# Performance work log

Hardware: AMD Instinct MI355X
Metric: run time of the kernel (lower is better)

Reference implementation:

```python
import jax, jax.numpy as jnp
import numpy as np

B, C, D, H, W = 2, 512, 32, 32, 32
L, CTX = 256, 768
NH, HD, G = 8, 64, 8
EPS = 1e-5


def group_norm(x, w, b):
    Bb, Cc, Dd, Hh, Ww = x.shape
    xg = x.reshape(Bb, G, Cc // G, Dd, Hh, Ww)
    mu = xg.mean(axis=(2, 3, 4, 5), keepdims=True)
    var = xg.var(axis=(2, 3, 4, 5), keepdims=True)
    xn = ((xg - mu) * jax.lax.rsqrt(var + EPS)).reshape(Bb, Cc, Dd, Hh, Ww)
    return xn * w[None, :, None, None, None] + b[None, :, None, None, None]


def layer_norm(x, w, b):
    mu = x.mean(axis=-1, keepdims=True)
    var = x.var(axis=-1, keepdims=True)
    return (x - mu) * jax.lax.rsqrt(var + EPS) * w + b


def setup_inputs() -> dict:
    key = jax.random.key(0)
    ks = jax.random.split(key, 8)
    s = 0.02  # weight init scale
    return {
        "x": jax.random.normal(ks[0], (B, C, D, H, W), jnp.float32),
        "context": jax.random.normal(ks[1], (B, L, CTX), jnp.float32),
        "gn_w": jnp.ones((C,), jnp.float32),
        "gn_b": jnp.zeros((C,), jnp.float32),
        "ln_w": jnp.ones((CTX,), jnp.float32),
        "ln_b": jnp.zeros((CTX,), jnp.float32),
        "q_w": jax.random.normal(ks[2], (C, C), jnp.float32) * s,
        "q_b": jnp.zeros((C,), jnp.float32),
        "k_w": jax.random.normal(ks[3], (C, CTX), jnp.float32) * s,
        "k_b": jnp.zeros((C,), jnp.float32),
        "v_w": jax.random.normal(ks[4], (C, CTX), jnp.float32) * s,
        "v_b": jnp.zeros((C,), jnp.float32),
        "proj_w": jax.random.normal(ks[5], (C, C), jnp.float32) * s,
        "proj_b": jnp.zeros((C,), jnp.float32),
    }


def reference(x, context, gn_w, gn_b, ln_w, ln_b, q_w, q_b, k_w, k_b, v_w, v_b, proj_w, proj_b):
    Bb, Cc, Dd, Hh, Ww = x.shape
    S = Dd * Hh * Ww
    h = group_norm(x, gn_w, gn_b)
    ctx = layer_norm(context, ln_w, ln_b)
    # 1x1 Conv3d == per-voxel linear over channels
    q = jnp.einsum('oc,bcdhw->bodhw', q_w, h) + q_b[None, :, None, None, None]
    q = q.reshape(Bb, NH, HD, S)                                        # (b,h,e,s)
    k = (ctx @ k_w.T + k_b).reshape(Bb, L, NH, HD).transpose(0, 2, 1, 3)  # (b,h,l,e)
    v = (ctx @ v_w.T + v_b).reshape(Bb, L, NH, HD).transpose(0, 2, 1, 3)  # (b,h,l,e)
    scale = HD ** -0.5
    attn = jnp.einsum('bhes,bhle->bhsl', q, k) * scale                  # (b,h,S,L)
    attn = jax.nn.softmax(attn, axis=-1)
    out = jnp.einsum('bhsl,bhle->bhes', attn, v).reshape(Bb, Cc, Dd, Hh, Ww)
    out = jnp.einsum('oc,bcdhw->bodhw', proj_w, out) + proj_b[None, :, None, None, None]
    return out + x
```

## Files before the change

### kernel.cpp

```cpp
#include <hip/hip_runtime.h>

typedef unsigned short u16;
typedef unsigned int u32;
typedef __attribute__((ext_vector_type(4))) float f32x4;
typedef __attribute__((ext_vector_type(8))) short bf16x8;
typedef __attribute__((ext_vector_type(8))) u16 u16x8;
typedef __attribute__((ext_vector_type(4))) u16 u16x4;
typedef __attribute__((ext_vector_type(4))) u32 u32x4;

#define DEVI __device__ __forceinline__

constexpr int C_ = 512, S_ = 32768, L_ = 256, CTX_ = 768;

DEVI u16 f2b(float f) {
    union { float f; unsigned u; } x; x.f = f;
    unsigned r = x.u + 0x7fffu + ((x.u >> 16) & 1u);
    return (u16)(r >> 16);
}

DEVI f32x4 mfma16(bf16x8 a, bf16x8 b, f32x4 c) {
    return __builtin_amdgcn_mfma_f32_16x16x32_bf16(a, b, c, 0, 0, 0);
}

DEVI void gload16(const void* g, void* l) {
    __builtin_amdgcn_global_load_lds(
        (const __attribute__((address_space(1))) void*)g,
        (__attribute__((address_space(3))) void*)l, 16, 0, 0);
}

DEVI u32 cvtpk(float lo, float hi) {
    u32 d;
    asm("v_cvt_pk_bf16_f32 %0, %1, %2" : "=v"(d) : "v"(lo), "v"(hi));
    return d;
}
DEVI void pl32(u32& a, u32& b) {
    asm volatile("v_permlane32_swap_b32 %0, %1" : "+v"(a), "+v"(b));
}
DEVI void pl16(u32& a, u32& b) {
    asm volatile("v_permlane16_swap_b32 %0, %1" : "+v"(a), "+v"(b));
}

__global__ __launch_bounds__(256) void cvt_w(
    const float* __restrict__ a0, const float* __restrict__ a1,
    const float* __restrict__ a2, const float* __restrict__ a3,
    u16* __restrict__ o0, u16* __restrict__ o1,
    u16* __restrict__ o2, u16* __restrict__ o3)
{
    int which = blockIdx.y;
    const float* src = which == 0 ? a0 : which == 1 ? a1 : which == 2 ? a2 : a3;
    u16* dst = which == 0 ? o0 : which == 1 ? o1 : which == 2 ? o2 : o3;
    int n4 = (which == 1 || which == 2) ? (512 * 768 / 4) : (512 * 512 / 4);
    int i = blockIdx.x * 256 + threadIdx.x;
    if (i < n4) {
        float4 v = ((const float4*)src)[i];
        u16x4 o; o[0] = f2b(v.x); o[1] = f2b(v.y); o[2] = f2b(v.z); o[3] = f2b(v.w);
        ((u16x4*)dst)[i] = o;
    }
}

__global__ __launch_bounds__(256) void gn_partial(const float* __restrict__ x,
                                                  float* __restrict__ part)
{
    const int bg = blockIdx.y, blk = blockIdx.x, tid = threadIdx.x;
    const float* base = x + (size_t)bg * 64 * S_ + (size_t)blk * 1024 + tid * 4;
    float s1 = 0.f, s2 = 0.f;
    for (int c = 0; c < 64; ++c) {
        float4 v = *(const float4*)(base + (size_t)c * S_);
        s1 += v.x + v.y + v.z + v.w;
        s2 += v.x * v.x + v.y * v.y + v.z * v.z + v.w * v.w;
    }
    for (int m = 1; m < 64; m <<= 1) { s1 += __shfl_xor(s1, m); s2 += __shfl_xor(s2, m); }
    __shared__ float a1[4], a2[4];
    int w = tid >> 6, lane = tid & 63;
    if (lane == 0) { a1[w] = s1; a2[w] = s2; }
    __syncthreads();
    if (tid == 0) {
        part[(bg * 32 + blk) * 2 + 0] = a1[0] + a1[1] + a1[2] + a1[3];
        part[(bg * 32 + blk) * 2 + 1] = a2[0] + a2[1] + a2[2] + a2[3];
    }
}

__global__ __launch_bounds__(64) void gn_final(const float* __restrict__ part,
                                               float* __restrict__ stats)
{
    int bg = blockIdx.x, tid = threadIdx.x;
    float s1 = tid < 32 ? part[(bg * 32 + tid) * 2] : 0.f;
    float s2 = tid < 32 ? part[(bg * 32 + tid) * 2 + 1] : 0.f;
    for (int m = 1; m < 32; m <<= 1) { s1 += __shfl_xor(s1, m); s2 += __shfl_xor(s2, m); }
    if (tid == 0) {
        const float invN = 1.0f / (64.0f * (float)S_);
        float mu = s1 * invN, var = s2 * invN - mu * mu;
        stats[bg * 2] = mu;
        stats[bg * 2 + 1] = rsqrtf(var + 1e-5f);
    }
}

__global__ __launch_bounds__(256) void gn_apply(
    const float* __restrict__ x, const float* __restrict__ stats,
    const float* __restrict__ gw, const float* __restrict__ gb,
    u16* __restrict__ ht)
{
    __shared__ float tile[64][65];
    const int tid = threadIdx.x, sl = tid & 63, c4 = tid >> 6;
    const int s0 = blockIdx.x * 64, c0 = blockIdx.y * 64, b = blockIdx.z;
    const int bg = b * 8 + (c0 >> 6);
    const float mu = stats[bg * 2], rstd = stats[bg * 2 + 1];
#pragma unroll
    for (int i = 0; i < 16; ++i) {
        int cl = c4 * 16 + i;
        float wv = gw[c0 + cl], bv = gb[c0 + cl];
        float v = x[((size_t)(b * C_ + c0 + cl)) * S_ + s0 + sl];
        tile[sl][cl] = (v - mu) * rstd * wv + bv;
    }
    __syncthreads();
#pragma unroll
    for (int rep = 0; rep < 2; ++rep) {
        int task = rep * 256 + tid;
        int so = task >> 3, cb = task & 7;
        u16x8 o;
#pragma unroll
        for (int j = 0; j < 8; ++j) o[j] = f2b(tile[so][cb * 8 + j]);
        *(u16x8*)&ht[((size_t)(b * S_ + s0 + so)) * C_ + c0 + cb * 8] = o;
    }
}

__global__ __launch_bounds__(256) void ln_ctx(
    const float* __restrict__ ctx, const float* __restrict__ lw,
    const float* __restrict__ lb, u16* __restrict__ cn)
{
    const int row = blockIdx.x, tid = threadIdx.x;
    const float* p = ctx + (size_t)row * CTX_;
    float v0 = p[tid], v1 = p[tid + 256], v2 = p[tid + 512];
    float s1 = v0 + v1 + v2, s2 = v0 * v0 + v1 * v1 + v2 * v2;
    for (int m = 1; m < 64; m <<= 1) { s1 += __shfl_xor(s1, m); s2 += __shfl_xor(s2, m); }
    __shared__ float a1[4], a2[4];
    int w = tid >> 6, lane = tid & 63;
    if (lane == 0) { a1[w] = s1; a2[w] = s2; }
    __syncthreads();
    s1 = a1[0] + a1[1] + a1[2] + a1[3];
    s2 = a2[0] + a2[1] + a2[2] + a2[3];
    const float invN = 1.0f / 768.0f;
    float mu = s1 * invN, rstd = rsqrtf(s2 * invN - mu * mu + 1e-5f);
    u16* o = cn + (size_t)row * CTX_;
    o[tid]       = f2b((v0 - mu) * rstd * lw[tid]       + lb[tid]);
    o[tid + 256] = f2b((v1 - mu) * rstd * lw[tid + 256] + lb[tid + 256]);
    o[tid + 512] = f2b((v2 - mu) * rstd * lw[tid + 512] + lb[tid + 512]);
}

template <int MODE, bool SWAP>
__global__ __launch_bounds__(256, 4) void gemm_nt(
    const u16* __restrict__ A, const u16* __restrict__ Bp,
    const float* __restrict__ bias, void* __restrict__ outp,
    const float* __restrict__ resid, int K, int ldo,
    size_t aStride, size_t bStride, size_t oStride, float scale,
    const u16* __restrict__ Bp2, const float* __restrict__ bias2,
    void* __restrict__ outp2)
{
    __shared__ __align__(16) u16 lA[2][4096];
    __shared__ __align__(16) u16 lB[2][4096];
    const int tid = threadIdx.x;
    const int w = tid >> 6, lane = tid & 63;
    const int g = lane >> 4, r = lane & 15;

    const int nx = gridDim.x, nxy = nx * gridDim.y;
    const int raw = blockIdx.x + nx * blockIdx.y;
    const int tile = (raw & 7) * (nxy >> 3) + (raw >> 3);
    const int bx = tile % nx, by = tile / nx;
    const int m0 = (SWAP ? by : bx) * 128, n0 = (SWAP ? bx : by) * 128;
    const int z = blockIdx.z;
    A += (size_t)z * aStride;
    const u16* Bsel = Bp;
    if constexpr (MODE == 3) { if (z) Bsel = Bp2; }
    Bsel += (size_t)z * bStride;

    const int l8 = lane & 7, lh = lane >> 3;
    const int u_ = l8 ^ lh;
    const int mro = (lh << 1) + (u_ >> 2);
    const int kco = (u_ & 3) * 8;
    const int wr = w >> 1, wc = w & 1;
    const int nt = K >> 5;

    f32x4 acc[4][4];
#pragma unroll
    for (int m = 0; m < 4; ++m)
#pragma unroll
        for (int n = 0; n < 4; ++n) acc[m][n] = f32x4{0.f, 0.f, 0.f, 0.f};

#define STAGE_T(t, bi_) {                                                      \
    size_t ko_ = (size_t)((t) * 32 + kco);                                     \
    _Pragma("unroll")                                                          \
    for (int j = 0; j < 2; ++j) {                                              \
        int grow_ = w * 32 + j * 16 + mro;                                     \
        gload16(A + (size_t)(m0 + grow_) * K + ko_,                            \
                &lA[bi_][(w * 16 + j * 8) << 6]);                              \
        gload16(Bsel + (size_t)(n0 + grow_) * K + ko_,                         \
                &lB[bi_][(w * 16 + j * 8) << 6]);                              \
    } }

    STAGE_T(0, 0);
    __syncthreads();

    for (int t = 0; t < nt; ++t) {
        const int cur = t & 1;
        if (t + 1 < nt) STAGE_T(t + 1, cur ^ 1);
        bf16x8 af[4], bf_[4];
#pragma unroll
        for (int m = 0; m < 4; ++m) {
            int row = wr * 32 + m * 8 + (r >> 1);
            int slot = (((r & 1) << 2) + g) ^ ((r >> 1) & 7);
            af[m] = *(const bf16x8*)&lA[cur][(row << 6) + (slot << 3)];
        }
#pragma unroll
        for (int n = 0; n < 4; ++n) {
            int row = wc * 32 + n * 8 + (r >> 1);
            int slot = (((r & 1) << 2) + g) ^ ((r >> 1) & 7);
            bf_[n] = *(const bf16x8*)&lB[cur][(row << 6) + (slot << 3)];
        }
#pragma unroll
        for (int m = 0; m < 4; ++m)
#pragma unroll
            for (int n = 0; n < 4; ++n)
                acc[m][n] = mfma16(bf_[n], af[m], acc[m][n]);
        __syncthreads();
    }
#undef STAGE_T

    if constexpr (MODE == 0) {
        u16* ob = (u16*)outp + (size_t)z * oStride;
#pragma unroll
        for (int m = 0; m < 4; ++m) {
            int gm = m0 + wr * 64 + m * 16 + r;
#pragma unroll
            for (int n = 0; n < 4; ++n) {
                int gn0 = n0 + wc * 64 + n * 16 + g * 4;
                float4 bn = *(const float4*)&bias[gn0];
                u32 w0 = cvtpk(acc[m][n][0] * scale + bn.x * scale,
                               acc[m][n][1] * scale + bn.y * scale);
                u32 w1 = cvtpk(acc[m][n][2] * scale + bn.z * scale,
                               acc[m][n][3] * scale + bn.w * scale);
                *(uint2*)&ob[(size_t)gm * ldo + gn0] = make_uint2(w0, w1);
            }
        }
    } else if constexpr (MODE == 2) {
        float* of = (float*)outp + (size_t)z * oStride;
        const float* rs = resid + (size_t)z * oStride;
#pragma unroll
        for (int m = 0; m < 4; ++m) {
            int gm = m0 + wr * 64 + m * 16 + r;
            float bm = bias[gm];
#pragma unroll
            for (int n = 0; n < 4; ++n) {
                int gn0 = n0 + wc * 64 + n * 16 + g * 4;
                size_t idx = (size_t)gm * ldo + gn0;
                float4 rv = *(const float4*)&rs[idx];
                float4 o4;
                o4.x = acc[m][n][0] + bm + rv.x;
                o4.y = acc[m][n][1] + bm + rv.y;
                o4.z = acc[m][n][2] + bm + rv.z;
                o4.w = acc[m][n][3] + bm + rv.w;
                *(float4*)&of[idx] = o4;
            }
        }
    } else if constexpr (MODE == 3) {
        if (z == 0) {
            u16* ob = (u16*)outp;
#pragma unroll
            for (int m = 0; m < 4; ++m) {
                int gm = m0 + wr * 64 + m * 16 + r;
#pragma unroll
                for (int n = 0; n < 4; ++n) {
                    int gn0 = n0 + wc * 64 + n * 16 + g * 4;
                    float4 bn = *(const float4*)&bias[gn0];
                    u32 w0 = cvtpk(acc[m][n][0] + bn.x, acc[m][n][1] + bn.y);
                    u32 w1 = cvtpk(acc[m][n][2] + bn.z, acc[m][n][3] + bn.w);
                    *(uint2*)&ob[(size_t)gm * ldo + gn0] = make_uint2(w0, w1);
                }
            }
        } else {
            u16* ob = (u16*)outp2;
#pragma unroll
            for (int m = 0; m < 4; ++m) {
                int gm = m0 + wr * 64 + m * 16 + r;
                int bb = gm >> 8, l = gm & 255;
#pragma unroll
                for (int n = 0; n < 4; ++n) {
                    int gn0 = n0 + wc * 64 + n * 16 + g * 4;
#pragma unroll
                    for (int i = 0; i < 4; ++i)
                        ob[((size_t)(bb * 512 + gn0 + i)) * 256 + l] =
                            f2b(acc[m][n][i] + bias2[gn0 + i]);
                }
            }
        }
    }
}

__global__ __launch_bounds__(256, 2) void attn_kernel(
    const u16* __restrict__ q, const u16* __restrict__ kk,
    const u16* __restrict__ vv, u16* __restrict__ ao)
{
    __shared__ __align__(16) u16 sm[32768];
    const int tid = threadIdx.x;
    const int w = tid >> 6, lane = tid & 63;
    const int g = lane >> 4, r = lane & 15;
    const int bh = blockIdx.y, b = bh >> 3, h = bh & 7;
    const int s0 = blockIdx.x * 128;

    {
        const u16* kbase = kk + ((size_t)b * L_) * C_ + h * 64;
#pragma unroll
        for (int j = 0; j < 8; ++j) {
            int idx = j * 256 + tid;
            int l = idx >> 3, ch = idx & 7;
            u16x8 val = *(const u16x8*)(kbase + (size_t)l * C_ + ch * 8);
            *(u16x8*)&sm[l * 64 + ((ch ^ (l & 7)) << 3)] = val;
        }
        const u16* vbase = vv + ((size_t)bh * 64) * 256;
#pragma unroll
        for (int j = 0; j < 8; ++j) {
            int idx = j * 256 + tid;
            int e = idx >> 5, ch = idx & 31;
            u16x8 val = *(const u16x8*)(vbase + (size_t)e * 256 + ch * 8);
            *(u16x8*)&sm[16384 + e * 256 + ((ch ^ (e & 7)) << 3)] = val;
        }
    }

    const int sw = s0 + w * 32;
    bf16x8 qf[2][2];
#pragma unroll
    for (int m = 0; m < 2; ++m)
#pragma unroll
        for (int kt = 0; kt < 2; ++kt)
            qf[m][kt] = *(const bf16x8*)(q + ((size_t)(b * S_ + sw + m * 16 + r)) * C_
                                         + h * 64 + kt * 32 + g * 8);
    __syncthreads();

    f32x4 accs[2][16];
#pragma unroll
    for (int m = 0; m < 2; ++m)
#pragma unroll
        for (int n = 0; n < 16; ++n) accs[m][n] = f32x4{0.f, 0.f, 0.f, 0.f};
    __builtin_amdgcn_s_setprio(1);
#pragma unroll
    for (int n = 0; n < 16; ++n) {
#pragma unroll
        for (int kt = 0; kt < 2; ++kt) {
            int c = kt * 4 + g;
            bf16x8 kf = *(const bf16x8*)&sm[(n * 16 + r) * 64 + ((c ^ (r & 7)) << 3)];
#pragma unroll
            for (int m = 0; m < 2; ++m) accs[m][n] = mfma16(kf, qf[m][kt], accs[m][n]);
        }
    }
    __builtin_amdgcn_s_setprio(0);

    float inv[2];
#pragma unroll
    for (int m = 0; m < 2; ++m) {
        float mx = accs[m][0][0];
#pragma unroll
        for (int n = 0; n < 16; ++n)
#pragma unroll
            for (int i = 0; i < 4; ++i) mx = fmaxf(mx, accs[m][n][i]);
        mx = fmaxf(mx, __shfl_xor(mx, 16));
        mx = fmaxf(mx, __shfl_xor(mx, 32));
        float sum = 0.f;
#pragma unroll
        for (int n = 0; n < 16; ++n)
#pragma unroll
            for (int i = 0; i < 4; ++i) {
                float e = __expf(accs[m][n][i] - mx);
                accs[m][n][i] = e; sum += e;
            }
        sum += __shfl_xor(sum, 16);
        sum += __shfl_xor(sum, 32);
        inv[m] = 1.0f / sum;
    }

    f32x4 acco[2][4];
#pragma unroll
    for (int m = 0; m < 2; ++m)
#pragma unroll
        for (int n = 0; n < 4; ++n) acco[m][n] = f32x4{0.f, 0.f, 0.f, 0.f};

#pragma unroll
    for (int c = 0; c < 8; ++c) {
        bf16x8 pa[2];
#pragma unroll
        for (int m = 0; m < 2; ++m) {
            u32 x0 = cvtpk(accs[m][2 * c][0] * inv[m], accs[m][2 * c][1] * inv[m]);
            u32 x1 = cvtpk(accs[m][2 * c][2] * inv[m], accs[m][2 * c][3] * inv[m]);
            u32 y0 = cvtpk(accs[m][2 * c + 1][0] * inv[m], accs[m][2 * c + 1][1] * inv[m]);
            u32 y1 = cvtpk(accs[m][2 * c + 1][2] * inv[m], accs[m][2 * c + 1][3] * inv[m]);
            pl32(x0, y0);
            pl32(x1, y1);
            pl16(x0, y0);
            pl16(x1, y1);
            u32x4 pw; pw[0] = x0; pw[1] = x1; pw[2] = y0; pw[3] = y1;
            pa[m] = *(bf16x8*)&pw;
        }
        bf16x8 vf[4];
#pragma unroll
        for (int n = 0; n < 4; ++n) {
            int e = n * 16 + r;
            vf[n] = *(const bf16x8*)&sm[16384 + e * 256 + (((c * 4 + g) ^ (r & 7)) << 3)];
        }
        __builtin_amdgcn_s_setprio(1);
#pragma unroll
        for (int m = 0; m < 2; ++m)
#pragma unroll
            for (int n = 0; n < 4; ++n)
                acco[m][n] = mfma16(vf[n], pa[m], acco[m][n]);
        __builtin_amdgcn_s_setprio(0);
    }

#pragma unroll
    for (int m = 0; m < 2; ++m) {
        const size_t rowb = ((size_t)(b * S_ + sw + m * 16 + r)) * C_ + h * 64;
#pragma unroll
        for (int n = 0; n < 4; ++n) {
            u32 w0 = cvtpk(acco[m][n][0], acco[m][n][1]);
            u32 w1 = cvtpk(acco[m][n][2], acco[m][n][3]);
            *(uint2*)&ao[rowb + n * 16 + g * 4] = make_uint2(w0, w1);
        }
    }
}

extern "C" void kernel_launch(void* const* d_in, const int* in_sizes, int n_in,
                              void* d_out, int out_size, void* d_ws, size_t ws_size,
                              hipStream_t stream)
{
    (void)in_sizes; (void)n_in; (void)out_size; (void)ws_size;
    const float* x    = (const float*)d_in[0];
    const float* ctx  = (const float*)d_in[1];
    const float* gn_w = (const float*)d_in[2];
    const float* gn_b = (const float*)d_in[3];
    const float* ln_w = (const float*)d_in[4];
    const float* ln_b = (const float*)d_in[5];
    const float* q_w  = (const float*)d_in[6];
    const float* q_b  = (const float*)d_in[7];
    const float* k_w  = (const float*)d_in[8];
    const float* k_b  = (const float*)d_in[9];
    const float* v_w  = (const float*)d_in[10];
    const float* v_b  = (const float*)d_in[11];
    const float* p_w  = (const float*)d_in[12];
    const float* p_b  = (const float*)d_in[13];
    float* out = (float*)d_out;

    char* ws = (char*)d_ws;
    constexpr size_t WS_WQ   = 0;
    constexpr size_t WS_WK   = WS_WQ + (size_t)512 * 512 * 2;
    constexpr size_t WS_WV   = WS_WK + (size_t)512 * 768 * 2;
    constexpr size_t WS_WP   = WS_WV + (size_t)512 * 768 * 2;
    constexpr size_t WS_PART = WS_WP + (size_t)512 * 512 * 2;
    constexpr size_t WS_STAT = WS_PART + (size_t)16 * 64 * 2 * 4;
    constexpr size_t WS_CTXN = WS_STAT + 256;
    constexpr size_t WS_K    = WS_CTXN + (size_t)512 * 768 * 2;
    constexpr size_t WS_V    = WS_K + (size_t)2 * 8 * 256 * 64 * 2;
    constexpr size_t WS_Q    = WS_V + (size_t)2 * 8 * 256 * 64 * 2;
    constexpr size_t WS_H    = WS_Q + (size_t)2 * 32768 * 512 * 2;

    u16* wq = (u16*)(ws + WS_WQ);
    u16* wk = (u16*)(ws + WS_WK);
    u16* wv = (u16*)(ws + WS_WV);
    u16* wp = (u16*)(ws + WS_WP);
    float* part  = (float*)(ws + WS_PART);
    float* stats = (float*)(ws + WS_STAT);
    u16* ctxn = (u16*)(ws + WS_CTXN);
    u16* kt   = (u16*)(ws + WS_K);
    u16* vt   = (u16*)(ws + WS_V);
    u16* qt   = (u16*)(ws + WS_Q);
    u16* ht   = (u16*)(ws + WS_H);
    u16* ao   = ht;

    const size_t bsc = (size_t)S_ * C_;

    cvt_w<<<dim3(384, 4), 256, 0, stream>>>(q_w, k_w, v_w, p_w, wq, wk, wv, wp);
    gn_partial<<<dim3(32, 16), 256, 0, stream>>>(x, part);
    gn_final<<<16, 64, 0, stream>>>(part, stats);
    gn_apply<<<dim3(512, 8, 2), 256, 0, stream>>>(x, stats, gn_w, gn_b, ht);
    ln_ctx<<<512, 256, 0, stream>>>(ctx, ln_w, ln_b, ctxn);
    gemm_nt<0, true><<<dim3(4, 256, 2), 256, 0, stream>>>(
        ht, wq, q_b, qt, nullptr, 512, 512, bsc, 0, bsc, 0.125f,
        nullptr, nullptr, nullptr);
    gemm_nt<3, false><<<dim3(4, 4, 2), 256, 0, stream>>>(
        ctxn, wk, k_b, kt, nullptr, 768, 512, 0, 0, 0, 1.0f,
        wv, v_b, vt);
    attn_kernel<<<dim3(256, 16), 256, 0, stream>>>(qt, kt, vt, ao);
    gemm_nt<2, false><<<dim3(4, 256, 2), 256, 0, stream>>>(
        wp, ao, p_b, out, x, 512, S_, 0, bsc, bsc, 1.0f,
        nullptr, nullptr, nullptr);
}
```

Baseline: 282.1 us.

## Fuse GroupNorm apply into Q projection GEMM A-operand load

Removes the gn_apply kernel that wrote a normalized, transposed bf16 copy of x. The Q GEMM now reads fp32 x directly and applies per-channel scale and shift coefficients from a tiny gn_coef kernel. It then converts to bf16 and writes the swizzled LDS tile, with the global loads issued ahead and the LDS writes done after the MFMAs. This saves a full write and re-read of the 32 MB intermediate, but the GEMM now loads fp32 data with register staging instead of async gload16, which may cost latency hiding.

```diff
diff --git a/kernel.cpp b/kernel.cpp
--- a/kernel.cpp
+++ b/kernel.cpp
@@ -95,33 +95,17 @@
     }
 }
 
-__global__ __launch_bounds__(256) void gn_apply(
-    const float* __restrict__ x, const float* __restrict__ stats,
-    const float* __restrict__ gw, const float* __restrict__ gb,
-    u16* __restrict__ ht)
-{
-    __shared__ float tile[64][65];
-    const int tid = threadIdx.x, sl = tid & 63, c4 = tid >> 6;
-    const int s0 = blockIdx.x * 64, c0 = blockIdx.y * 64, b = blockIdx.z;
-    const int bg = b * 8 + (c0 >> 6);
-    const float mu = stats[bg * 2], rstd = stats[bg * 2 + 1];
-#pragma unroll
-    for (int i = 0; i < 16; ++i) {
-        int cl = c4 * 16 + i;
-        float wv = gw[c0 + cl], bv = gb[c0 + cl];
-        float v = x[((size_t)(b * C_ + c0 + cl)) * S_ + s0 + sl];
-        tile[sl][cl] = (v - mu) * rstd * wv + bv;
-    }
-    __syncthreads();
-#pragma unroll
-    for (int rep = 0; rep < 2; ++rep) {
-        int task = rep * 256 + tid;
-        int so = task >> 3, cb = task & 7;
-        u16x8 o;
-#pragma unroll
-        for (int j = 0; j < 8; ++j) o[j] = f2b(tile[so][cb * 8 + j]);
-        *(u16x8*)&ht[((size_t)(b * S_ + s0 + so)) * C_ + c0 + cb * 8] = o;
-    }
+__global__ __launch_bounds__(256) void gn_coef(
+    const float* __restrict__ stats, const float* __restrict__ gw,
+    const float* __restrict__ gb, float* __restrict__ ca, float* __restrict__ cb)
+{
+    int i = blockIdx.x * 256 + threadIdx.x;
+    int z = i >> 9, c = i & 511;
+    int bg = z * 8 + (c >> 6);
+    float mu = stats[bg * 2], rs = stats[bg * 2 + 1];
+    float a = rs * gw[c];
+    ca[i] = a;
+    cb[i] = gb[c] - mu * a;
 }
 
 __global__ __launch_bounds__(256) void ln_ctx(
@@ -186,23 +170,76 @@
 #pragma unroll
         for (int n = 0; n < 4; ++n) acc[m][n] = f32x4{0.f, 0.f, 0.f, 0.f};
 
-#define STAGE_T(t, bi_) {                                                      \
+#define STAGE_B(t, bi_) {                                                      \
+    size_t ko_ = (size_t)((t) * 32 + kco);                                     \
+    _Pragma("unroll")                                                          \
+    for (int j = 0; j < 2; ++j) {                                              \
+        int grow_ = w * 32 + j * 16 + mro;                                     \
+        gload16(Bsel + (size_t)(n0 + grow_) * K + ko_,                         \
+                &lB[bi_][(w * 16 + j * 8) << 6]);                              \
+    } }
+
+#define STAGE_A(t, bi_) {                                                      \
     size_t ko_ = (size_t)((t) * 32 + kco);                                     \
     _Pragma("unroll")                                                          \
     for (int j = 0; j < 2; ++j) {                                              \
         int grow_ = w * 32 + j * 16 + mro;                                     \
         gload16(A + (size_t)(m0 + grow_) * K + ko_,                            \
                 &lA[bi_][(w * 16 + j * 8) << 6]);                              \
-        gload16(Bsel + (size_t)(n0 + grow_) * K + ko_,                         \
-                &lB[bi_][(w * 16 + j * 8) << 6]);                              \
     } }
 
-    STAGE_T(0, 0);
+    const float* xA = nullptr;
+    const float* cAp = nullptr;
+    const float* cBp = nullptr;
+    int cp2 = 0, sb = 0, zc = 0;
+    f32x4 a00{}, a01{}, a10{}, a11{};
+    float2 ka{}, kb{};
+    if constexpr (MODE == 4) {
+        xA = resid + (size_t)z * ((size_t)C_ * S_);
+        cAp = bias2;
+        cBp = (const float*)outp2;
+        cp2 = (tid >> 4) * 2;
+        sb = (tid & 15) * 8;
+        zc = z * 512;
+    }
+
+#define LOAD_A4(t) {                                                           \
+    int c0n_ = (t) * 32 + cp2;                                                 \
+    const float* r0_ = xA + (size_t)c0n_ * S_ + m0 + sb;                       \
+    a00 = *(const f32x4*)r0_;  a01 = *(const f32x4*)(r0_ + 4);                 \
+    a10 = *(const f32x4*)(r0_ + S_); a11 = *(const f32x4*)(r0_ + S_ + 4);      \
+    ka = *(const float2*)&cAp[zc + c0n_];                                      \
+    kb = *(const float2*)&cBp[zc + c0n_]; }
+
+#define WRITE_A4(bi_) {                                                        \
+    _Pragma("unroll")                                                          \
+    for (int j = 0; j < 8; ++j) {                                              \
+        float v0_ = ((j < 4) ? a00[j] : a01[j - 4]) * ka.x + kb.x;             \
+        float v1_ = ((j < 4) ? a10[j] : a11[j - 4]) * ka.y + kb.y;             \
+        int mm_ = sb + j;                                                      \
+        int idx_ = ((mm_ >> 1) << 6)                                           \
+            + (((((mm_ & 1) << 2) + (cp2 >> 3)) ^ ((mm_ >> 1) & 7)) << 3)      \
+            + (cp2 & 7);                                                       \
+        *(u32*)&lA[bi_][idx_] = cvtpk(v0_, v1_);                               \
+    } }
+
+    if constexpr (MODE == 4) {
+        STAGE_B(0, 0);
+        LOAD_A4(0);
+        WRITE_A4(0);
+    } else {
+        STAGE_A(0, 0);
+        STAGE_B(0, 0);
+    }
     __syncthreads();
 
     for (int t = 0; t < nt; ++t) {
         const int cur = t & 1;
-        if (t + 1 < nt) STAGE_T(t + 1, cur ^ 1);
+        if (t + 1 < nt) {
+            STAGE_B(t + 1, cur ^ 1);
+            if constexpr (MODE == 4) { LOAD_A4(t + 1); }
+            else                     { STAGE_A(t + 1, cur ^ 1); }
+        }
         bf16x8 af[4], bf_[4];
 #pragma unroll
         for (int m = 0; m < 4; ++m) {
@@ -221,11 +258,15 @@
 #pragma unroll
             for (int n = 0; n < 4; ++n)
                 acc[m][n] = mfma16(bf_[n], af[m], acc[m][n]);
+        if constexpr (MODE == 4) { if (t + 1 < nt) WRITE_A4(cur ^ 1); }
         __syncthreads();
     }
-#undef STAGE_T
-
-    if constexpr (MODE == 0) {
+#undef STAGE_A
+#undef STAGE_B
+#undef LOAD_A4
+#undef WRITE_A4
+
+    if constexpr (MODE == 0 || MODE == 4) {
         u16* ob = (u16*)outp + (size_t)z * oStride;
 #pragma unroll
         for (int m = 0; m < 4; ++m) {
@@ -453,7 +494,9 @@
     constexpr size_t WS_WP   = WS_WV + (size_t)512 * 768 * 2;
     constexpr size_t WS_PART = WS_WP + (size_t)512 * 512 * 2;
     constexpr size_t WS_STAT = WS_PART + (size_t)16 * 64 * 2 * 4;
-    constexpr size_t WS_CTXN = WS_STAT + 256;
+    constexpr size_t WS_CA   = WS_STAT + 256;
+    constexpr size_t WS_CB   = WS_CA + 4096;
+    constexpr size_t WS_CTXN = WS_CB + 4096;
     constexpr size_t WS_K    = WS_CTXN + (size_t)512 * 768 * 2;
     constexpr size_t WS_V    = WS_K + (size_t)2 * 8 * 256 * 64 * 2;
     constexpr size_t WS_Q    = WS_V + (size_t)2 * 8 * 256 * 64 * 2;
@@ -465,23 +508,24 @@
     u16* wp = (u16*)(ws + WS_WP);
     float* part  = (float*)(ws + WS_PART);
     float* stats = (float*)(ws + WS_STAT);
+    float* coefA = (float*)(ws + WS_CA);
+    float* coefB = (float*)(ws + WS_CB);
     u16* ctxn = (u16*)(ws + WS_CTXN);
     u16* kt   = (u16*)(ws + WS_K);
     u16* vt   = (u16*)(ws + WS_V);
     u16* qt   = (u16*)(ws + WS_Q);
-    u16* ht   = (u16*)(ws + WS_H);
-    u16* ao   = ht;
+    u16* ao   = (u16*)(ws + WS_H);
 
     const size_t bsc = (size_t)S_ * C_;
 
     cvt_w<<<dim3(384, 4), 256, 0, stream>>>(q_w, k_w, v_w, p_w, wq, wk, wv, wp);
     gn_partial<<<dim3(32, 16), 256, 0, stream>>>(x, part);
     gn_final<<<16, 64, 0, stream>>>(part, stats);
-    gn_apply<<<dim3(512, 8, 2), 256, 0, stream>>>(x, stats, gn_w, gn_b, ht);
+    gn_coef<<<4, 256, 0, stream>>>(stats, gn_w, gn_b, coefA, coefB);
     ln_ctx<<<512, 256, 0, stream>>>(ctx, ln_w, ln_b, ctxn);
-    gemm_nt<0, true><<<dim3(4, 256, 2), 256, 0, stream>>>(
-        ht, wq, q_b, qt, nullptr, 512, 512, bsc, 0, bsc, 0.125f,
-        nullptr, nullptr, nullptr);
+    gemm_nt<4, true><<<dim3(4, 256, 2), 256, 0, stream>>>(
+        nullptr, wq, q_b, qt, x, 512, 512, 0, 0, bsc, 0.125f,
+        nullptr, coefA, coefB);
     gemm_nt<3, false><<<dim3(4, 4, 2), 256, 0, stream>>>(
         ctxn, wk, k_b, kt, nullptr, 768, 512, 0, 0, 0, 1.0f,
         wv, v_b, vt);
```

After: 273.6 us. 1.03x faster.
